# Kernel tuning notes

Measured on AMD Instinct MI355X. Metric: run time of the kernel, lower is better.

Reference implementation:

```python
import jax, jax.numpy as jnp
import numpy as np

N_NODES = 512
IN_FEATURES = 512
N_HEADS = 8
N_HIDDEN = 64  # out_features // n_heads
NEG_SLOPE = 0.2


def setup_inputs() -> dict:
    key = jax.random.key(0)
    k_h, k_ws, k_wt, k_a, k_adj = jax.random.split(key, 5)
    lim_w = 1.0 / np.sqrt(IN_FEATURES)
    lim_a = 1.0 / np.sqrt(N_HIDDEN)
    h = jax.random.normal(k_h, (1, N_NODES, IN_FEATURES), dtype=jnp.float32)
    # nn.Linear weights: [out, in]
    W_source = jax.random.uniform(k_ws, (N_HEADS * N_HIDDEN, IN_FEATURES), jnp.float32, -lim_w, lim_w)
    W_target = jax.random.uniform(k_wt, (N_HEADS * N_HIDDEN, IN_FEATURES), jnp.float32, -lim_w, lim_w)
    attn_w = jax.random.uniform(k_a, (N_HIDDEN,), jnp.float32, -lim_a, lim_a)  # Linear(n_hidden, 1)
    adjacency_matrix = jax.random.randint(k_adj, (N_NODES, N_NODES, 1), 0, 2, dtype=jnp.int32)
    return {"h": h, "W_source": W_source, "W_target": W_target,
            "attn_w": attn_w, "adjacency_matrix": adjacency_matrix}


def reference(h, W_source, W_target, attn_w, adjacency_matrix):
    n_nodes = h.shape[1]
    x = h[0]  # [N, D]; module assumes batch == 1
    g_source = (x @ W_source.T).reshape(n_nodes, N_HEADS, N_HIDDEN)  # [N,H,F]
    g_target = (x @ W_target.T).reshape(n_nodes, N_HEADS, N_HIDDEN)  # [N,H,F]
    # g_sum[i, j] = g_source[j] + g_target[i]  (repeat / repeat_interleave semantics)
    g_sum = g_source[None, :, :, :] + g_target[:, None, :, :]  # [N,N,H,F]
    act = jnp.where(g_sum >= 0, g_sum, NEG_SLOPE * g_sum)       # LeakyReLU
    scores = jnp.einsum('ijhf,f->ijh', act, attn_w)              # [N,N,H]
    scores = jnp.where(adjacency_matrix == 0, -jnp.inf, scores)  # adj broadcasts over heads
    attention = jax.nn.softmax(scores, axis=1)                   # softmax over source nodes j
    # dropout p applied at eval -> identity
    head_output = jnp.einsum('ijh,jhf->ihf', attention, g_target)  # [N,H,F]
    out = head_output.reshape(n_nodes, N_HEADS * N_HIDDEN)         # is_concat=True
    return out, attention
```

## Files before the change

kernel.cpp:

```cpp
#include <hip/hip_runtime.h>

#define NN 512
#define IND 512
#define NH 8
#define NF 64

__global__ __launch_bounds__(256) void gemm_nt(
    const float* __restrict__ Aa, const float* __restrict__ Ba, float* __restrict__ Ca,
    const float* __restrict__ Ab, const float* __restrict__ Bb, float* __restrict__ Cb)
{
    const float* A = blockIdx.z ? Ab : Aa;
    const float* B = blockIdx.z ? Bb : Ba;
    float*       C = blockIdx.z ? Cb : Ca;

    __shared__ __align__(16) float Vs[2][32][132];
    __shared__ float2 sp[2][4][64];

    const int tid  = threadIdx.x;
    const int wv   = __builtin_amdgcn_readfirstlane(tid >> 6);
    const int lane = tid & 63;
    const int rg = wv & 1, kh = wv >> 1;
    const int r0 = blockIdx.y * 8 + rg * 4;
    const int c0 = blockIdx.x * 128;

    const float* Sp = A + (size_t)r0 * IND + kh * 256;
    const int ts = tid & 127;
    const float* Brow = B + (size_t)(c0 + ts) * IND + kh * 256;

    float2 a0 = {0.f,0.f}, a1 = {0.f,0.f}, a2 = {0.f,0.f}, a3 = {0.f,0.f};

    for (int ch = 0; ch < 8; ++ch) {
        float4 f[8];
        const float4* bp = reinterpret_cast<const float4*>(Brow + ch * 32);
        #pragma unroll
        for (int i = 0; i < 8; ++i) f[i] = bp[i];
        __syncthreads();
        #pragma unroll
        for (int i = 0; i < 8; ++i) {
            Vs[kh][i * 4 + 0][ts] = f[i].x;
            Vs[kh][i * 4 + 1][ts] = f[i].y;
            Vs[kh][i * 4 + 2][ts] = f[i].z;
            Vs[kh][i * 4 + 3][ts] = f[i].w;
        }
        __syncthreads();
        const float* Spc = Sp + ch * 32;
        #pragma unroll 8
        for (int kk = 0; kk < 32; ++kk) {
            float2 v = *reinterpret_cast<const float2*>(&Vs[kh][kk][lane * 2]);
            float s0 = Spc[kk];
            float s1 = Spc[IND + kk];
            float s2 = Spc[2 * IND + kk];
            float s3 = Spc[3 * IND + kk];
            a0.x = fmaf(s0, v.x, a0.x); a0.y = fmaf(s0, v.y, a0.y);
            a1.x = fmaf(s1, v.x, a1.x); a1.y = fmaf(s1, v.y, a1.y);
            a2.x = fmaf(s2, v.x, a2.x); a2.y = fmaf(s2, v.y, a2.y);
            a3.x = fmaf(s3, v.x, a3.x); a3.y = fmaf(s3, v.y, a3.y);
        }
    }

    if (kh) {
        sp[rg][0][lane] = a0; sp[rg][1][lane] = a1;
        sp[rg][2][lane] = a2; sp[rg][3][lane] = a3;
    }
    __syncthreads();
    if (!kh) {
        float2 p;
        const int cc = c0 + lane * 2;
        p = sp[rg][0][lane]; a0.x += p.x; a0.y += p.y;
        p = sp[rg][1][lane]; a1.x += p.x; a1.y += p.y;
        p = sp[rg][2][lane]; a2.x += p.x; a2.y += p.y;
        p = sp[rg][3][lane]; a3.x += p.x; a3.y += p.y;
        *reinterpret_cast<float2*>(C + (size_t)(r0 + 0) * NN + cc) = a0;
        *reinterpret_cast<float2*>(C + (size_t)(r0 + 1) * NN + cc) = a1;
        *reinterpret_cast<float2*>(C + (size_t)(r0 + 2) * NN + cc) = a2;
        *reinterpret_cast<float2*>(C + (size_t)(r0 + 3) * NN + cc) = a3;
    }
}

__global__ __launch_bounds__(256) void gat_attn(
    const float* __restrict__ Gs_t,
    const float* __restrict__ Gt,
    const float* __restrict__ attn_w,
    const int*   __restrict__ adj,
    float* __restrict__ out_feat,
    float* __restrict__ att_ws)
{
    __shared__ float s_sc[4][512];
    __shared__ float s_red[4][4][64];

    const int tid = threadIdx.x;
    const int i0  = blockIdx.x * 4;
    const int h   = blockIdx.y;

    {
        const int jj = tid * 2;
        float2 acc0 = {0.f,0.f}, acc1 = {0.f,0.f}, acc2 = {0.f,0.f}, acc3 = {0.f,0.f};
        float2 p = {0.f,0.f};
        const float* gsp = Gs_t + (size_t)h * NF * NN + jj;
        const float* gtp = Gt + (size_t)i0 * IND + h * NF;
        #pragma unroll 4
        for (int f = 0; f < NF; ++f) {
            float w  = attn_w[f];
            float2 g = *reinterpret_cast<const float2*>(gsp + (size_t)f * NN);
            float gt0 = gtp[f];
            float gt1 = gtp[IND + f];
            float gt2 = gtp[2 * IND + f];
            float gt3 = gtp[3 * IND + f];
            p.x = fmaf(w, g.x, p.x);
            p.y = fmaf(w, g.y, p.y);
            float tx, ty;
            tx = g.x + gt0; ty = g.y + gt0;
            acc0.x = fmaf(w, fabsf(tx), acc0.x); acc0.y = fmaf(w, fabsf(ty), acc0.y);
            tx = g.x + gt1; ty = g.y + gt1;
            acc1.x = fmaf(w, fabsf(tx), acc1.x); acc1.y = fmaf(w, fabsf(ty), acc1.y);
            tx = g.x + gt2; ty = g.y + gt2;
            acc2.x = fmaf(w, fabsf(tx), acc2.x); acc2.y = fmaf(w, fabsf(ty), acc2.y);
            tx = g.x + gt3; ty = g.y + gt3;
            acc3.x = fmaf(w, fabsf(tx), acc3.x); acc3.y = fmaf(w, fabsf(ty), acc3.y);
        }
        const float px = 0.6f * p.x, py = 0.6f * p.y;
        int2 ad;
        ad = *reinterpret_cast<const int2*>(adj + (size_t)(i0 + 0) * NN + jj);
        s_sc[0][jj]     = ad.x ? fmaf(0.4f, acc0.x, px) : -INFINITY;
        s_sc[0][jj + 1] = ad.y ? fmaf(0.4f, acc0.y, py) : -INFINITY;
        ad = *reinterpret_cast<const int2*>(adj + (size_t)(i0 + 1) * NN + jj);
        s_sc[1][jj]     = ad.x ? fmaf(0.4f, acc1.x, px) : -INFINITY;
        s_sc[1][jj + 1] = ad.y ? fmaf(0.4f, acc1.y, py) : -INFINITY;
        ad = *reinterpret_cast<const int2*>(adj + (size_t)(i0 + 2) * NN + jj);
        s_sc[2][jj]     = ad.x ? fmaf(0.4f, acc2.x, px) : -INFINITY;
        s_sc[2][jj + 1] = ad.y ? fmaf(0.4f, acc2.y, py) : -INFINITY;
        ad = *reinterpret_cast<const int2*>(adj + (size_t)(i0 + 3) * NN + jj);
        s_sc[3][jj]     = ad.x ? fmaf(0.4f, acc3.x, px) : -INFINITY;
        s_sc[3][jj + 1] = ad.y ? fmaf(0.4f, acc3.y, py) : -INFINITY;
    }
    __syncthreads();

    {
        const int ii = tid >> 6, lane = tid & 63;
        float m = -INFINITY;
        #pragma unroll
        for (int r = 0; r < 8; ++r) m = fmaxf(m, s_sc[ii][lane + r * 64]);
        #pragma unroll
        for (int off = 32; off >= 1; off >>= 1) m = fmaxf(m, __shfl_xor(m, off, 64));
        float e[8];
        float sum = 0.f;
        #pragma unroll
        for (int r = 0; r < 8; ++r) {
            float ev = __expf(s_sc[ii][lane + r * 64] - m);
            e[r] = ev;
            sum += ev;
        }
        #pragma unroll
        for (int off = 32; off >= 1; off >>= 1) sum += __shfl_xor(sum, off, 64);
        float inv = 1.f / sum;
        const int i = i0 + ii;
        float* awp = att_ws + ((size_t)h * NN + i) * NN;
        #pragma unroll
        for (int r = 0; r < 8; ++r) {
            int j = lane + r * 64;
            float a = e[r] * inv;
            s_sc[ii][j] = a;
            awp[j] = a;
        }
    }
    __syncthreads();

    {
        const int w = tid >> 6, lane = tid & 63;
        const int jb = w * 128;
        float o0 = 0.f, o1 = 0.f, o2 = 0.f, o3 = 0.f;
        const float* gtc = Gt + h * NF + lane;
        #pragma unroll 4
        for (int s = 0; s < 32; ++s) {
            const int j = jb + 4 * s;
            float4 b0 = *reinterpret_cast<const float4*>(&s_sc[0][j]);
            float4 b1 = *reinterpret_cast<const float4*>(&s_sc[1][j]);
            float4 b2 = *reinterpret_cast<const float4*>(&s_sc[2][j]);
            float4 b3 = *reinterpret_cast<const float4*>(&s_sc[3][j]);
            float gv;
            gv = gtc[(size_t)(j + 0) * IND];
            o0 = fmaf(b0.x, gv, o0); o1 = fmaf(b1.x, gv, o1);
            o2 = fmaf(b2.x, gv, o2); o3 = fmaf(b3.x, gv, o3);
            gv = gtc[(size_t)(j + 1) * IND];
            o0 = fmaf(b0.y, gv, o0); o1 = fmaf(b1.y, gv, o1);
            o2 = fmaf(b2.y, gv, o2); o3 = fmaf(b3.y, gv, o3);
            gv = gtc[(size_t)(j + 2) * IND];
            o0 = fmaf(b0.z, gv, o0); o1 = fmaf(b1.z, gv, o1);
            o2 = fmaf(b2.z, gv, o2); o3 = fmaf(b3.z, gv, o3);
            gv = gtc[(size_t)(j + 3) * IND];
            o0 = fmaf(b0.w, gv, o0); o1 = fmaf(b1.w, gv, o1);
            o2 = fmaf(b2.w, gv, o2); o3 = fmaf(b3.w, gv, o3);
        }
        s_red[w][0][lane] = o0; s_red[w][1][lane] = o1;
        s_red[w][2][lane] = o2; s_red[w][3][lane] = o3;
    }
    __syncthreads();
    {
        const int ii = tid >> 6, f = tid & 63;
        float s = s_red[0][ii][f] + s_red[1][ii][f] + s_red[2][ii][f] + s_red[3][ii][f];
        out_feat[(size_t)(i0 + ii) * (NH * NF) + h * NF + f] = s;
    }
}

__global__ __launch_bounds__(256) void att_pack(
    const float* __restrict__ att_ws, float* __restrict__ out_att)
{
    const int tid = threadIdx.x;
    const int i0  = blockIdx.x * 2;
    const int jj  = tid * 2;
    #pragma unroll
    for (int ii = 0; ii < 2; ++ii) {
        const int i = i0 + ii;
        float2 v[8];
        #pragma unroll
        for (int h = 0; h < 8; ++h)
            v[h] = *reinterpret_cast<const float2*>(att_ws + ((size_t)h * NN + i) * NN + jj);
        float4* dst = reinterpret_cast<float4*>(out_att + ((size_t)i * NN + jj) * NH);
        float4 o;
        o.x = v[0].x; o.y = v[1].x; o.z = v[2].x; o.w = v[3].x; dst[0] = o;
        o.x = v[4].x; o.y = v[5].x; o.z = v[6].x; o.w = v[7].x; dst[1] = o;
        o.x = v[0].y; o.y = v[1].y; o.z = v[2].y; o.w = v[3].y; dst[2] = o;
        o.x = v[4].y; o.y = v[5].y; o.z = v[6].y; o.w = v[7].y; dst[3] = o;
    }
}

extern "C" void kernel_launch(void* const* d_in, const int* in_sizes, int n_in,
                              void* d_out, int out_size, void* d_ws, size_t ws_size,
                              hipStream_t stream) {
    const float* X   = (const float*)d_in[0];
    const float* Ws  = (const float*)d_in[1];
    const float* Wtg = (const float*)d_in[2];
    const float* aw  = (const float*)d_in[3];
    const int*   adj = (const int*)d_in[4];

    float* Gs_t   = (float*)d_ws;
    float* Gt     = Gs_t   + (size_t)NN * IND;
    float* att_ws = Gt     + (size_t)NN * IND;

    float* out_feat = (float*)d_out;
    float* out_att  = out_feat + (size_t)NN * NH * NF;

    hipLaunchKernelGGL(gemm_nt, dim3(4, 64, 2), dim3(256), 0, stream,
                       Ws, X, Gs_t, X, Wtg, Gt);
    hipLaunchKernelGGL(gat_attn, dim3(NN / 4, NH), dim3(256), 0, stream,
                       Gs_t, Gt, aw, adj, out_feat, att_ws);
    hipLaunchKernelGGL(att_pack, dim3(NN / 2), dim3(256), 0, stream,
                       att_ws, out_att);
}
```

Measured before the change: 110.1 us.

## Fuse attention transpose into gat_attn and process eight rows per block

Drops the separate att_pack kernel and the att_ws staging buffer: the attention kernel now writes probabilities straight into the interleaved [i][j][h] output layout. The block grows to 512 threads handling 8 target rows per head instead of 4, with one source column per thread, so Gs_t and Gt loads are reused across more rows. This removes a kernel launch and a round trip through global memory. The cost is strided scalar stores (stride 8 floats) for the attention output, a 2x smaller grid (512 blocks), and higher register and shared-memory use per block.

```diff
diff --git a/kernel.cpp b/kernel.cpp
--- a/kernel.cpp
+++ b/kernel.cpp
@@ -77,150 +77,116 @@
     }
 }
 
-__global__ __launch_bounds__(256) void gat_attn(
+__global__ __launch_bounds__(512) void gat_attn(
     const float* __restrict__ Gs_t,
     const float* __restrict__ Gt,
     const float* __restrict__ attn_w,
     const int*   __restrict__ adj,
     float* __restrict__ out_feat,
-    float* __restrict__ att_ws)
+    float* __restrict__ out_att)
 {
-    __shared__ float s_sc[4][512];
-    __shared__ float s_red[4][4][64];
+    __shared__ float s_sc[8][512];
+    __shared__ float s_red[8][8][64];
 
     const int tid = threadIdx.x;
-    const int i0  = blockIdx.x * 4;
+    const int i0  = blockIdx.x * 8;
     const int h   = blockIdx.y;
 
     {
-        const int jj = tid * 2;
-        float2 acc0 = {0.f,0.f}, acc1 = {0.f,0.f}, acc2 = {0.f,0.f}, acc3 = {0.f,0.f};
-        float2 p = {0.f,0.f};
-        const float* gsp = Gs_t + (size_t)h * NF * NN + jj;
+        const int j = tid;
+        float acc[8];
+        #pragma unroll
+        for (int i = 0; i < 8; ++i) acc[i] = 0.f;
+        float p = 0.f;
+        const float* gsp = Gs_t + (size_t)h * NF * NN + j;
         const float* gtp = Gt + (size_t)i0 * IND + h * NF;
         #pragma unroll 4
         for (int f = 0; f < NF; ++f) {
-            float w  = attn_w[f];
-            float2 g = *reinterpret_cast<const float2*>(gsp + (size_t)f * NN);
-            float gt0 = gtp[f];
-            float gt1 = gtp[IND + f];
-            float gt2 = gtp[2 * IND + f];
-            float gt3 = gtp[3 * IND + f];
-            p.x = fmaf(w, g.x, p.x);
-            p.y = fmaf(w, g.y, p.y);
-            float tx, ty;
-            tx = g.x + gt0; ty = g.y + gt0;
-            acc0.x = fmaf(w, fabsf(tx), acc0.x); acc0.y = fmaf(w, fabsf(ty), acc0.y);
-            tx = g.x + gt1; ty = g.y + gt1;
-            acc1.x = fmaf(w, fabsf(tx), acc1.x); acc1.y = fmaf(w, fabsf(ty), acc1.y);
-            tx = g.x + gt2; ty = g.y + gt2;
-            acc2.x = fmaf(w, fabsf(tx), acc2.x); acc2.y = fmaf(w, fabsf(ty), acc2.y);
-            tx = g.x + gt3; ty = g.y + gt3;
-            acc3.x = fmaf(w, fabsf(tx), acc3.x); acc3.y = fmaf(w, fabsf(ty), acc3.y);
-        }
-        const float px = 0.6f * p.x, py = 0.6f * p.y;
-        int2 ad;
-        ad = *reinterpret_cast<const int2*>(adj + (size_t)(i0 + 0) * NN + jj);
-        s_sc[0][jj]     = ad.x ? fmaf(0.4f, acc0.x, px) : -INFINITY;
-        s_sc[0][jj + 1] = ad.y ? fmaf(0.4f, acc0.y, py) : -INFINITY;
-        ad = *reinterpret_cast<const int2*>(adj + (size_t)(i0 + 1) * NN + jj);
-        s_sc[1][jj]     = ad.x ? fmaf(0.4f, acc1.x, px) : -INFINITY;
-        s_sc[1][jj + 1] = ad.y ? fmaf(0.4f, acc1.y, py) : -INFINITY;
-        ad = *reinterpret_cast<const int2*>(adj + (size_t)(i0 + 2) * NN + jj);
-        s_sc[2][jj]     = ad.x ? fmaf(0.4f, acc2.x, px) : -INFINITY;
-        s_sc[2][jj + 1] = ad.y ? fmaf(0.4f, acc2.y, py) : -INFINITY;
-        ad = *reinterpret_cast<const int2*>(adj + (size_t)(i0 + 3) * NN + jj);
-        s_sc[3][jj]     = ad.x ? fmaf(0.4f, acc3.x, px) : -INFINITY;
-        s_sc[3][jj + 1] = ad.y ? fmaf(0.4f, acc3.y, py) : -INFINITY;
-    }
-    __syncthreads();
-
-    {
-        const int ii = tid >> 6, lane = tid & 63;
+            float w = attn_w[f];
+            float g = gsp[(size_t)f * NN];
+            p = fmaf(w, g, p);
+            #pragma unroll
+            for (int i = 0; i < 8; ++i) {
+                float t = g + gtp[(size_t)i * IND + f];
+                acc[i] = fmaf(w, fabsf(t), acc[i]);
+            }
+        }
+        const float px = 0.6f * p;
+        #pragma unroll
+        for (int i = 0; i < 8; ++i) {
+            int ad = adj[(size_t)(i0 + i) * NN + j];
+            s_sc[i][j] = ad ? fmaf(0.4f, acc[i], px) : -INFINITY;
+        }
+    }
+    __syncthreads();
+
+    {
+        const int w = tid >> 6, lane = tid & 63;
         float m = -INFINITY;
         #pragma unroll
-        for (int r = 0; r < 8; ++r) m = fmaxf(m, s_sc[ii][lane + r * 64]);
+        for (int r = 0; r < 8; ++r) m = fmaxf(m, s_sc[w][lane + r * 64]);
         #pragma unroll
         for (int off = 32; off >= 1; off >>= 1) m = fmaxf(m, __shfl_xor(m, off, 64));
         float e[8];
         float sum = 0.f;
         #pragma unroll
         for (int r = 0; r < 8; ++r) {
-            float ev = __expf(s_sc[ii][lane + r * 64] - m);
+            float ev = __expf(s_sc[w][lane + r * 64] - m);
             e[r] = ev;
             sum += ev;
         }
         #pragma unroll
         for (int off = 32; off >= 1; off >>= 1) sum += __shfl_xor(sum, off, 64);
         float inv = 1.f / sum;
-        const int i = i0 + ii;
-        float* awp = att_ws + ((size_t)h * NN + i) * NN;
+        const int i = i0 + w;
         #pragma unroll
         for (int r = 0; r < 8; ++r) {
             int j = lane + r * 64;
             float a = e[r] * inv;
-            s_sc[ii][j] = a;
-            awp[j] = a;
+            s_sc[w][j] = a;
+            out_att[((size_t)i * NN + j) * NH + h] = a;
         }
     }
     __syncthreads();
 
     {
         const int w = tid >> 6, lane = tid & 63;
-        const int jb = w * 128;
-        float o0 = 0.f, o1 = 0.f, o2 = 0.f, o3 = 0.f;
+        const int jb = w * 64;
+        float o[8];
+        #pragma unroll
+        for (int i = 0; i < 8; ++i) o[i] = 0.f;
         const float* gtc = Gt + h * NF + lane;
-        #pragma unroll 4
-        for (int s = 0; s < 32; ++s) {
+        #pragma unroll 2
+        for (int s = 0; s < 16; ++s) {
             const int j = jb + 4 * s;
-            float4 b0 = *reinterpret_cast<const float4*>(&s_sc[0][j]);
-            float4 b1 = *reinterpret_cast<const float4*>(&s_sc[1][j]);
-            float4 b2 = *reinterpret_cast<const float4*>(&s_sc[2][j]);
-            float4 b3 = *reinterpret_cast<const float4*>(&s_sc[3][j]);
+            float4 b[8];
+            #pragma unroll
+            for (int i = 0; i < 8; ++i)
+                b[i] = *reinterpret_cast<const float4*>(&s_sc[i][j]);
             float gv;
             gv = gtc[(size_t)(j + 0) * IND];
-            o0 = fmaf(b0.x, gv, o0); o1 = fmaf(b1.x, gv, o1);
-            o2 = fmaf(b2.x, gv, o2); o3 = fmaf(b3.x, gv, o3);
+            #pragma unroll
+            for (int i = 0; i < 8; ++i) o[i] = fmaf(b[i].x, gv, o[i]);
             gv = gtc[(size_t)(j + 1) * IND];
-            o0 = fmaf(b0.y, gv, o0); o1 = fmaf(b1.y, gv, o1);
-            o2 = fmaf(b2.y, gv, o2); o3 = fmaf(b3.y, gv, o3);
+            #pragma unroll
+            for (int i = 0; i < 8; ++i) o[i] = fmaf(b[i].y, gv, o[i]);
             gv = gtc[(size_t)(j + 2) * IND];
-            o0 = fmaf(b0.z, gv, o0); o1 = fmaf(b1.z, gv, o1);
-            o2 = fmaf(b2.z, gv, o2); o3 = fmaf(b3.z, gv, o3);
+            #pragma unroll
+            for (int i = 0; i < 8; ++i) o[i] = fmaf(b[i].z, gv, o[i]);
             gv = gtc[(size_t)(j + 3) * IND];
-            o0 = fmaf(b0.w, gv, o0); o1 = fmaf(b1.w, gv, o1);
-            o2 = fmaf(b2.w, gv, o2); o3 = fmaf(b3.w, gv, o3);
-        }
-        s_red[w][0][lane] = o0; s_red[w][1][lane] = o1;
-        s_red[w][2][lane] = o2; s_red[w][3][lane] = o3;
+            #pragma unroll
+            for (int i = 0; i < 8; ++i) o[i] = fmaf(b[i].w, gv, o[i]);
+        }
+        #pragma unroll
+        for (int i = 0; i < 8; ++i) s_red[w][i][lane] = o[i];
     }
     __syncthreads();
     {
         const int ii = tid >> 6, f = tid & 63;
-        float s = s_red[0][ii][f] + s_red[1][ii][f] + s_red[2][ii][f] + s_red[3][ii][f];
+        float s = 0.f;
+        #pragma unroll
+        for (int w = 0; w < 8; ++w) s += s_red[w][ii][f];
         out_feat[(size_t)(i0 + ii) * (NH * NF) + h * NF + f] = s;
-    }
-}
-
-__global__ __launch_bounds__(256) void att_pack(
-    const float* __restrict__ att_ws, float* __restrict__ out_att)
-{
-    const int tid = threadIdx.x;
-    const int i0  = blockIdx.x * 2;
-    const int jj  = tid * 2;
-    #pragma unroll
-    for (int ii = 0; ii < 2; ++ii) {
-        const int i = i0 + ii;
-        float2 v[8];
-        #pragma unroll
-        for (int h = 0; h < 8; ++h)
-            v[h] = *reinterpret_cast<const float2*>(att_ws + ((size_t)h * NN + i) * NN + jj);
-        float4* dst = reinterpret_cast<float4*>(out_att + ((size_t)i * NN + jj) * NH);
-        float4 o;
-        o.x = v[0].x; o.y = v[1].x; o.z = v[2].x; o.w = v[3].x; dst[0] = o;
-        o.x = v[4].x; o.y = v[5].x; o.z = v[6].x; o.w = v[7].x; dst[1] = o;
-        o.x = v[0].y; o.y = v[1].y; o.z = v[2].y; o.w = v[3].y; dst[2] = o;
-        o.x = v[4].y; o.y = v[5].y; o.z = v[6].y; o.w = v[7].y; dst[3] = o;
     }
 }
 
@@ -233,17 +199,14 @@
     const float* aw  = (const float*)d_in[3];
     const int*   adj = (const int*)d_in[4];
 
-    float* Gs_t   = (float*)d_ws;
-    float* Gt     = Gs_t   + (size_t)NN * IND;
-    float* att_ws = Gt     + (size_t)NN * IND;
+    float* Gs_t = (float*)d_ws;
+    float* Gt   = Gs_t + (size_t)NN * IND;
 
     float* out_feat = (float*)d_out;
     float* out_att  = out_feat + (size_t)NN * NH * NF;
 
     hipLaunchKernelGGL(gemm_nt, dim3(4, 64, 2), dim3(256), 0, stream,
                        Ws, X, Gs_t, X, Wtg, Gt);
-    hipLaunchKernelGGL(gat_attn, dim3(NN / 4, NH), dim3(256), 0, stream,
-                       Gs_t, Gt, aw, adj, out_feat, att_ws);
-    hipLaunchKernelGGL(att_pack, dim3(NN / 2), dim3(256), 0, stream,
-                       att_ws, out_att);
+    hipLaunchKernelGGL(gat_attn, dim3(NN / 8, NH), dim3(512), 0, stream,
+                       Gs_t, Gt, aw, adj, out_feat, out_att);
 }
```

Measured after the change: 107.2 us. -2.7%, faster.
